# Kernel tuning notes

Hardware: AMD Instinct MI355X
Metric: run time of the kernel (lower is better)

## Reference

```python
import jax, jax.numpy as jnp
import numpy as np

N_NODES = 4096
N_EDGES = 8192
N_GRAPHS = 256
D_NODE = 64
D_EDGE = 32
H = 256


def setup_inputs() -> dict:
    key = jax.random.key(0)
    ks = jax.random.split(key, 16)
    s = lambda d: 1.0 / np.sqrt(d)
    inp = {
        "x": jax.random.normal(ks[0], (N_NODES, D_NODE), dtype=jnp.float32),
        "edge_index": jax.random.randint(ks[1], (2, N_EDGES), 0, N_NODES),
        "edge_attr": jax.random.normal(ks[2], (N_EDGES, D_EDGE), dtype=jnp.float32),
        "batch": jnp.sort(jax.random.randint(ks[3], (N_NODES,), 0, N_GRAPHS)),
        # conv1: edge MLP 32 -> 64*256, root weight 64->256, bias 256
        "nn1_w": jax.random.normal(ks[4], (D_EDGE, D_NODE * H), dtype=jnp.float32) * s(D_EDGE),
        "nn1_b": jnp.zeros((D_NODE * H,), dtype=jnp.float32),
        "root1_w": jax.random.normal(ks[5], (D_NODE, H), dtype=jnp.float32) * s(D_NODE),
        "bias1": jnp.zeros((H,), dtype=jnp.float32),
        # conv2: edge MLP 32 -> 256*256, root weight 256->256, bias 256
        "nn2_w": jax.random.normal(ks[6], (D_EDGE, H * H), dtype=jnp.float32) * s(D_EDGE),
        "nn2_b": jnp.zeros((H * H,), dtype=jnp.float32),
        "root2_w": jax.random.normal(ks[7], (H, H), dtype=jnp.float32) * s(H),
        "bias2": jnp.zeros((H,), dtype=jnp.float32),
        # readout MLP: 256 -> 128 -> 1
        "lin1_w": jax.random.normal(ks[8], (H, H // 2), dtype=jnp.float32) * s(H),
        "lin1_b": jnp.zeros((H // 2,), dtype=jnp.float32),
        "lin2_w": jax.random.normal(ks[9], (H // 2, 1), dtype=jnp.float32) * s(H // 2),
        "lin2_b": jnp.zeros((1,), dtype=jnp.float32),
    }
    return inp


def nnconv(x, src, dst, edge_attr, nn_w, nn_b, root_w, bias, out_c):
    # PyG NNConv (aggr='add'): per-edge weight matrix from edge MLP,
    # message = x[src] @ W_e, scatter-add at dst, plus root transform + bias.
    e = edge_attr.shape[0]
    in_c = x.shape[1]
    w_e = (edge_attr @ nn_w + nn_b).reshape(e, in_c, out_c)  # [E, in, out]
    msg = jnp.einsum('ei,eio->eo', x[src], w_e)              # [E, out]
    agg = jax.ops.segment_sum(msg, dst, num_segments=x.shape[0])
    return agg + x @ root_w + bias


def reference(x, edge_index, edge_attr, batch,
              nn1_w, nn1_b, root1_w, bias1,
              nn2_w, nn2_b, root2_w, bias2,
              lin1_w, lin1_b, lin2_w, lin2_b):
    src, dst = edge_index[0], edge_index[1]
    h = nnconv(x, src, dst, edge_attr, nn1_w, nn1_b, root1_w, bias1, H)
    h = jax.nn.relu(h)
    h = nnconv(h, src, dst, edge_attr, nn2_w, nn2_b, root2_w, bias2, H)
    # global mean pool over graphs
    sums = jax.ops.segment_sum(h, batch, num_segments=N_GRAPHS)
    cnts = jax.ops.segment_sum(jnp.ones((h.shape[0],), h.dtype), batch, num_segments=N_GRAPHS)
    pooled = sums / jnp.maximum(cnts, 1.0)[:, None]
    # dropout is identity in eval mode
    z = jax.nn.relu(pooled @ lin1_w + lin1_b)
    return jax.nn.sigmoid(z @ lin2_w + lin2_b)  # [N_GRAPHS, 1]
```

## Files before the change

kernel.cpp:

```cpp
#include <hip/hip_runtime.h>
#include <math.h>

#define N_NODES 4096
#define N_EDGES 8192
#define N_GRAPHS 256
#define D_NODE 64
#define D_EDGE 32
#define HH 256

#define K1 2176
#define K2 8704
#define NC1 34
#define NC2 136
#define NSL1 8
#define NSL3 32
#define CHUNK 64

typedef _Float16 half8v __attribute__((ext_vector_type(8)));
typedef _Float16 half4v __attribute__((ext_vector_type(4)));
typedef float floatx4 __attribute__((ext_vector_type(4)));

static const size_t OFF_S    = 0;
static const size_t OFF_BT1  = 17825792;
static const size_t OFF_BT2  = 18104320;
static const size_t OFF_CP   = 19218432;
static const size_t OFF_H    = 25509888;
static const size_t OFF_INT  = 26034176;
static const size_t OFF_POOL = 26050560;

__device__ void csr_body(const int* __restrict__ dst,
                         int* __restrict__ starts,
                         int* __restrict__ elist) {
    __shared__ int cnt[4096];
    __shared__ int ps[256];
    int t = threadIdx.x;
#pragma unroll
    for (int i = 0; i < 16; ++i) cnt[t * 16 + i] = 0;
    __syncthreads();
#pragma unroll
    for (int i = 0; i < 32; ++i) atomicAdd(&cnt[dst[i * 256 + t]], 1);
    __syncthreads();
    int v[16]; int s = 0;
#pragma unroll
    for (int i = 0; i < 16; ++i) { v[i] = cnt[t * 16 + i]; s += v[i]; }
    ps[t] = s;
    __syncthreads();
    for (int off = 1; off < 256; off <<= 1) {
        int tv = (t >= off) ? ps[t - off] : 0;
        __syncthreads();
        ps[t] += tv;
        __syncthreads();
    }
    int excl = ps[t] - s;
#pragma unroll
    for (int i = 0; i < 16; ++i) {
        starts[t * 16 + i] = excl;
        cnt[t * 16 + i] = excl;
        excl += v[i];
    }
    if (t == 255) starts[4096] = excl;
    __syncthreads();
#pragma unroll
    for (int i = 0; i < 32; ++i) {
        int e = i * 256 + t;
        int d = dst[e];
        int p = atomicAdd(&cnt[d], 1);
        elist[p] = e;
    }
}

__device__ void gstarts_body(const int* __restrict__ batch, int* __restrict__ gstarts) {
    int t = threadIdx.x;
    int lo = 0, hi = N_NODES;
    while (lo < hi) { int mid = (lo + hi) >> 1; if (batch[mid] < t) lo = mid + 1; else hi = mid; }
    gstarts[t] = lo;
    if (t == 0) gstarts[N_GRAPHS] = N_NODES;
}

__device__ void packT_body(const float* __restrict__ w,
                           const float* __restrict__ b,
                           const float* __restrict__ rw,
                           _Float16* __restrict__ BT,
                           int kk0, int o0, int K,
                           int wlim, int blim, int wshift, int wmask, int wrow) {
    __shared__ float T[64][65];
    int t = threadIdx.x;
    int ol = t & 63, kb = t >> 6;
#pragma unroll
    for (int p = 0; p < 16; ++p) {
        int kl = p * 4 + kb;
        int kk = kk0 + kl, o = o0 + ol;
        float v;
        if (kk < wlim)      v = w[(kk >> wshift) * wrow + (kk & wmask) * 256 + o];
        else if (kk < blim) v = b[(kk - wlim) * 256 + o];
        else                v = rw[(kk - blim) * 256 + o];
        T[kl][ol] = v;
    }
    __syncthreads();
    int kl2 = t & 63, ob = t >> 6;
#pragma unroll
    for (int p = 0; p < 16; ++p) {
        int ol2 = p * 4 + ob;
        BT[(size_t)(o0 + ol2) * K + kk0 + kl2] = (_Float16)T[kl2][ol2];
    }
}

__global__ __launch_bounds__(256) void prep_k(const int* __restrict__ dst,
                                              const int* __restrict__ batch,
                                              int* __restrict__ starts,
                                              int* __restrict__ elist,
                                              int* __restrict__ gstarts,
                                              const float* __restrict__ w1,
                                              const float* __restrict__ b1,
                                              const float* __restrict__ r1,
                                              const float* __restrict__ w2,
                                              const float* __restrict__ b2,
                                              const float* __restrict__ r2,
                                              _Float16* __restrict__ BT1,
                                              _Float16* __restrict__ BT2) {
    int bx = blockIdx.x, by = blockIdx.y;
    if (bx == 0) {
        if (by == 0) csr_body(dst, starts, elist);
        else if (by == 1) gstarts_body(batch, gstarts);
        return;
    }
    int pbx = bx - 1, o0 = by * 64;
    if (pbx < NC1)
        packT_body(w1, b1, r1, BT1, pbx * 64, o0, K1, 2048, 2112, 6, 63, 16384);
    else
        packT_body(w2, b2, r2, BT2, (pbx - NC1) * 64, o0, K2, 8192, 8448, 8, 255, 65536);
}

__global__ __launch_bounds__(256) void s1_k(const float* __restrict__ x,
                                            const float* __restrict__ ea,
                                            const int* __restrict__ src,
                                            const int* __restrict__ starts,
                                            const int* __restrict__ elist,
                                            _Float16* __restrict__ S) {
    int t = threadIdx.x;
    int n = blockIdx.x * 4 + (t >> 6);
    int tl = t & 63;
    int cg = tl & 7, kg = tl >> 3;
    int i0 = cg * 8;
    float acc[5][8] = {};
    int e0 = starts[n], e1 = starts[n + 1];
    for (int ie = e0; ie < e1; ++ie) {
        int e = elist[ie];
        int sn = src[e];
        float4 f0 = *(const float4*)&x[sn * 64 + i0];
        float4 f1 = *(const float4*)&x[sn * 64 + i0 + 4];
        float xv[8] = {f0.x, f0.y, f0.z, f0.w, f1.x, f1.y, f1.z, f1.w};
#pragma unroll
        for (int j = 0; j < 4; ++j) {
            float va = ea[e * 32 + kg + 8 * j];
#pragma unroll
            for (int c = 0; c < 8; ++c) acc[j][c] += va * xv[c];
        }
        if (kg == 0) {
#pragma unroll
            for (int c = 0; c < 8; ++c) acc[4][c] += xv[c];
        }
    }
    _Float16* row = S + (size_t)n * K1;
#pragma unroll
    for (int j = 0; j < 4; ++j) {
        int k = kg + 8 * j;
        half8v o;
#pragma unroll
        for (int c = 0; c < 8; ++c) o[c] = (_Float16)acc[j][c];
        *(half8v*)&row[k * 64 + i0] = o;
    }
    if (kg == 0) {
        half8v o;
#pragma unroll
        for (int c = 0; c < 8; ++c) o[c] = (_Float16)acc[4][c];
        *(half8v*)&row[32 * 64 + i0] = o;
    }
    if (kg == 1) {
        float4 f0 = *(const float4*)&x[n * 64 + i0];
        float4 f1 = *(const float4*)&x[n * 64 + i0 + 4];
        half8v o;
        o[0] = (_Float16)f0.x; o[1] = (_Float16)f0.y; o[2] = (_Float16)f0.z; o[3] = (_Float16)f0.w;
        o[4] = (_Float16)f1.x; o[5] = (_Float16)f1.y; o[6] = (_Float16)f1.z; o[7] = (_Float16)f1.w;
        *(half8v*)&row[2112 + i0] = o;
    }
}

__device__ __forceinline__ void async_copy16(const void* g, void* l) {
    __builtin_amdgcn_global_load_lds(
        (__attribute__((address_space(1))) unsigned int*)(g),
        (__attribute__((address_space(3))) unsigned int*)(l), 16, 0, 0);
}

__global__ __launch_bounds__(256, 3) void gemm_f16(const _Float16* __restrict__ A,
                                                   const _Float16* __restrict__ BT,
                                                   _Float16* __restrict__ Cpart,
                                                   int K, int NC, int Z) {
    __shared__ _Float16 lds[17408];
    _Float16* As = lds;
    _Float16* Bs = lds + 128 * 64;
    int tid = threadIdx.x;
    int w = tid >> 6, l = tid & 63;
    int mt = blockIdx.y, nt = blockIdx.x, z = blockIdx.z;
    int c0 = z * NC / Z, c1 = (z + 1) * NC / Z;
    int k0 = c0 * 64;
    int wm = w & 1, wn = w >> 1;

    int lr = l >> 3, lc = l & 7;
    int gc = lc ^ lr;
    const _Float16* gA0 = A  + (size_t)(mt * 128 + w * 32 + lr) * K + k0 + gc * 8;
    const _Float16* gB0 = BT + (size_t)(nt * 128 + w * 32 + lr) * K + k0 + gc * 8;

    int lm = l & 15, q4 = l >> 4;
    int sw = lm & 7;

    floatx4 acc[4][4] = {};

    for (int s = c0; s < c1; ++s) {
#pragma unroll
        for (int q = 0; q < 4; ++q) {
            async_copy16(gA0 + (size_t)q * 8 * K, As + (w * 32 + q * 8) * 64);
            async_copy16(gB0 + (size_t)q * 8 * K, Bs + (w * 32 + q * 8) * 64);
        }
        gA0 += 64; gB0 += 64;
        __syncthreads();
#pragma unroll
        for (int kw = 0; kw < 2; ++kw) {
            int ck = ((kw * 4 + q4) ^ sw) * 8;
            half8v af[4], bf[4];
#pragma unroll
            for (int i = 0; i < 4; ++i)
                af[i] = *(const half8v*)&As[(wm * 64 + i * 16 + lm) * 64 + ck];
#pragma unroll
            for (int j = 0; j < 4; ++j)
                bf[j] = *(const half8v*)&Bs[(wn * 64 + j * 16 + lm) * 64 + ck];
#pragma unroll
            for (int i = 0; i < 4; ++i)
#pragma unroll
                for (int j = 0; j < 4; ++j)
                    acc[i][j] = __builtin_amdgcn_mfma_f32_16x16x32_f16(af[i], bf[j], acc[i][j], 0, 0, 0);
        }
        __syncthreads();
    }

    _Float16* ep = lds + w * 4352;
#pragma unroll
    for (int i = 0; i < 4; ++i)
#pragma unroll
        for (int j = 0; j < 4; ++j)
#pragma unroll
            for (int r = 0; r < 4; ++r)
                ep[(i * 16 + q4 * 4 + r) * 68 + j * 16 + lm] = (_Float16)acc[i][j][r];
    __syncthreads();
    _Float16* Cp = Cpart + (size_t)z * (N_NODES * HH);
    int row8 = l >> 3, colg = (l & 7) * 8;
    int gm0 = mt * 128 + wm * 64, gn0 = nt * 128 + wn * 64;
#pragma unroll
    for (int i8 = 0; i8 < 8; ++i8) {
        int rr = i8 * 8 + row8;
        half4v lo = *(const half4v*)&ep[rr * 68 + colg];
        half4v hi = *(const half4v*)&ep[rr * 68 + colg + 4];
        half8v v;
        v[0] = lo[0]; v[1] = lo[1]; v[2] = lo[2]; v[3] = lo[3];
        v[4] = hi[0]; v[5] = hi[1]; v[6] = hi[2]; v[7] = hi[3];
        *(half8v*)&Cp[(size_t)(gm0 + rr) * HH + gn0 + colg] = v;
    }
}

__global__ __launch_bounds__(256) void hep_k(const _Float16* __restrict__ Cp,
                                             const float* __restrict__ bias,
                                             _Float16* __restrict__ h,
                                             float* __restrict__ pool) {
    if (blockIdx.x < 256) pool[blockIdx.x * 256 + threadIdx.x] = 0.f;
    int idx = (blockIdx.x * 256 + threadIdx.x) * 8;
    float a[8] = {};
#pragma unroll
    for (int zz = 0; zz < NSL1; ++zz) {
        half8v v = *(const half8v*)(Cp + (size_t)zz * (N_NODES * HH) + idx);
#pragma unroll
        for (int j = 0; j < 8; ++j) a[j] += (float)v[j];
    }
    int col = idx & 255;
    half8v o;
#pragma unroll
    for (int j = 0; j < 8; ++j) o[j] = (_Float16)fmaxf(a[j] + bias[col + j], 0.f);
    *(half8v*)(h + idx) = o;
}

__global__ __launch_bounds__(256) void sg_k(const _Float16* __restrict__ h,
                                            const float* __restrict__ ea,
                                            const int* __restrict__ src,
                                            const int* __restrict__ starts,
                                            const int* __restrict__ elist,
                                            const int* __restrict__ gstarts,
                                            _Float16* __restrict__ SG) {
    int g = blockIdx.x, ks = blockIdx.y, t = threadIdx.x;
    __shared__ int sl[CHUNK];
    __shared__ int el[CHUNK];
    __shared__ float eaS[CHUNK * 32];
    int nlo = gstarts[g], nhi = gstarts[g + 1];
    int e0 = starts[nlo], e1 = starts[nhi];
    _Float16* row = SG + (size_t)g * K2;
    int kbase = ks * 16;

    float acc[16] = {};
    float a32 = 0.f;
    for (int base = e0; base < e1; base += CHUNK) {
        int ne = min(CHUNK, e1 - base);
        if (t < ne) { int e = elist[base + t]; el[t] = e; sl[t] = src[e]; }
        __syncthreads();
        for (int j = t; j < ne * 32; j += 256)
            eaS[j] = ea[(size_t)el[j >> 5] * 32 + (j & 31)];
        __syncthreads();
        int ie = 0;
        for (; ie + 4 <= ne; ie += 4) {
            float hv[4];
#pragma unroll
            for (int u = 0; u < 4; ++u) hv[u] = (float)h[(size_t)sl[ie + u] * 256 + t];
#pragma unroll
            for (int u = 0; u < 4; ++u) {
                const float* er = &eaS[(ie + u) * 32 + kbase];
#pragma unroll
                for (int q = 0; q < 4; ++q) {
                    float4 ev = *(const float4*)&er[q * 4];
                    acc[q * 4 + 0] += ev.x * hv[u]; acc[q * 4 + 1] += ev.y * hv[u];
                    acc[q * 4 + 2] += ev.z * hv[u]; acc[q * 4 + 3] += ev.w * hv[u];
                }
                if (ks == 1) a32 += hv[u];
            }
        }
        for (; ie < ne; ++ie) {
            float hv = (float)h[(size_t)sl[ie] * 256 + t];
            const float* er = &eaS[ie * 32 + kbase];
#pragma unroll
            for (int q = 0; q < 4; ++q) {
                float4 ev = *(const float4*)&er[q * 4];
                acc[q * 4 + 0] += ev.x * hv; acc[q * 4 + 1] += ev.y * hv;
                acc[q * 4 + 2] += ev.z * hv; acc[q * 4 + 3] += ev.w * hv;
            }
            if (ks == 1) a32 += hv;
        }
        __syncthreads();
    }
#pragma unroll
    for (int j = 0; j < 16; ++j)
        row[(kbase + j) * 256 + t] = (_Float16)acc[j];
    if (ks == 1) {
        float aug = 0.f;
        int n = nlo;
        for (; n + 4 <= nhi; n += 4) {
            float hv[4];
#pragma unroll
            for (int u = 0; u < 4; ++u) hv[u] = (float)h[(size_t)(n + u) * 256 + t];
#pragma unroll
            for (int u = 0; u < 4; ++u) aug += hv[u];
        }
        for (; n < nhi; ++n) aug += (float)h[(size_t)n * 256 + t];
        row[32 * 256 + t] = (_Float16)a32;
        row[8448 + t] = (_Float16)aug;
    }
}

__global__ __launch_bounds__(256, 3) void gemm_sg(const _Float16* __restrict__ A,
                                                  const _Float16* __restrict__ BT,
                                                  float* __restrict__ pool,
                                                  int K, int NC, int Z) {
    __shared__ _Float16 lds[16384];
    _Float16* As = lds;
    _Float16* Bs = lds + 128 * 64;
    int tid = threadIdx.x;
    int w = tid >> 6, l = tid & 63;
    int mt = blockIdx.y, nt = blockIdx.x, z = blockIdx.z;
    int c0 = z * NC / Z, c1 = (z + 1) * NC / Z;
    int k0 = c0 * 64;
    int wm = w & 1, wn = w >> 1;

    int lr = l >> 3, lc = l & 7;
    int gc = lc ^ lr;
    const _Float16* gA0 = A  + (size_t)(mt * 128 + w * 32 + lr) * K + k0 + gc * 8;
    const _Float16* gB0 = BT + (size_t)(nt * 128 + w * 32 + lr) * K + k0 + gc * 8;

    int lm = l & 15, q4 = l >> 4;
    int sw = lm & 7;

    floatx4 acc[4][4] = {};

    for (int s = c0; s < c1; ++s) {
#pragma unroll
        for (int q = 0; q < 4; ++q) {
            async_copy16(gA0 + (size_t)q * 8 * K, As + (w * 32 + q * 8) * 64);
            async_copy16(gB0 + (size_t)q * 8 * K, Bs + (w * 32 + q * 8) * 64);
        }
        gA0 += 64; gB0 += 64;
        __syncthreads();
#pragma unroll
        for (int kw = 0; kw < 2; ++kw) {
            int ck = ((kw * 4 + q4) ^ sw) * 8;
            half8v af[4], bf[4];
#pragma unroll
            for (int i = 0; i < 4; ++i)
                af[i] = *(const half8v*)&As[(wm * 64 + i * 16 + lm) * 64 + ck];
#pragma unroll
            for (int j = 0; j < 4; ++j)
                bf[j] = *(const half8v*)&Bs[(wn * 64 + j * 16 + lm) * 64 + ck];
#pragma unroll
            for (int i = 0; i < 4; ++i)
#pragma unroll
                for (int j = 0; j < 4; ++j)
                    acc[i][j] = __builtin_amdgcn_mfma_f32_16x16x32_f16(af[i], bf[j], acc[i][j], 0, 0, 0);
        }
        __syncthreads();
    }

    int gm0 = mt * 128 + wm * 64, gn0 = nt * 128 + wn * 64;
#pragma unroll
    for (int i = 0; i < 4; ++i)
#pragma unroll
        for (int j = 0; j < 4; ++j)
#pragma unroll
            for (int r = 0; r < 4; ++r)
                atomicAdd(&pool[(size_t)(gm0 + i * 16 + q4 * 4 + r) * HH + gn0 + j * 16 + lm],
                          acc[i][j][r]);
}

__global__ __launch_bounds__(256) void readout_k(const float* __restrict__ pool,
                                                 const int* __restrict__ gstarts,
                                                 const float* __restrict__ bias2,
                                                 const float* __restrict__ l1w,
                                                 const float* __restrict__ l1b,
                                                 const float* __restrict__ l2w,
                                                 const float* __restrict__ l2b,
                                                 float* __restrict__ out) {
    int g = blockIdx.x, t = threadIdx.x;
    __shared__ float sp[256];
    __shared__ float sz[128];
    int lo = gstarts[g], hi = gstarts[g + 1];
    sp[t] = (hi > lo) ? (pool[g * 256 + t] / (float)(hi - lo) + bias2[t]) : 0.f;
    __syncthreads();
    if (t < 128) {
        float a = l1b[t];
#pragma unroll 8
        for (int i = 0; i < 256; ++i) a += sp[i] * l1w[i * 128 + t];
        sz[t] = fmaxf(a, 0.f) * l2w[t];
    }
    __syncthreads();
    for (int ss = 64; ss > 0; ss >>= 1) {
        if (t < ss) sz[t] += sz[t + ss];
        __syncthreads();
    }
    if (t == 0) {
        float zz = sz[0] + l2b[0];
        out[g] = 1.0f / (1.0f + expf(-zz));
    }
}

extern "C" void kernel_launch(void* const* d_in, const int* in_sizes, int n_in,
                              void* d_out, int out_size, void* d_ws, size_t ws_size,
                              hipStream_t stream) {
    const float* x       = (const float*)d_in[0];
    const int*   ei      = (const int*)d_in[1];
    const float* ea      = (const float*)d_in[2];
    const int*   batch   = (const int*)d_in[3];
    const float* nn1_w   = (const float*)d_in[4];
    const float* nn1_b   = (const float*)d_in[5];
    const float* root1_w = (const float*)d_in[6];
    const float* bias1   = (const float*)d_in[7];
    const float* nn2_w   = (const float*)d_in[8];
    const float* nn2_b   = (const float*)d_in[9];
    const float* root2_w = (const float*)d_in[10];
    const float* bias2   = (const float*)d_in[11];
    const float* lin1_w  = (const float*)d_in[12];
    const float* lin1_b  = (const float*)d_in[13];
    const float* lin2_w  = (const float*)d_in[14];
    const float* lin2_b  = (const float*)d_in[15];
    float* out = (float*)d_out;
    float* ws  = (float*)d_ws;

    _Float16* S   = (_Float16*)(ws + OFF_S);
    _Float16* BT1 = (_Float16*)(ws + OFF_BT1);
    _Float16* BT2 = (_Float16*)(ws + OFF_BT2);
    _Float16* Cp  = (_Float16*)(ws + OFF_CP);
    _Float16* h   = (_Float16*)(ws + OFF_H);
    int* ip      = (int*)(ws + OFF_INT);
    int* starts  = ip;
    int* elist   = ip + 4100;
    int* gstarts = ip + 12292;
    float* pool  = ws + OFF_POOL;

    const int* srcv = ei;
    const int* dstv = ei + N_EDGES;

    prep_k<<<dim3(1 + NC1 + NC2, 4), 256, 0, stream>>>(
        dstv, batch, starts, elist, gstarts,
        nn1_w, nn1_b, root1_w, nn2_w, nn2_b, root2_w, BT1, BT2);

    s1_k<<<1024, 256, 0, stream>>>(x, ea, srcv, starts, elist, S);

    gemm_f16<<<dim3(2, 32, NSL1), 256, 0, stream>>>(S, BT1, Cp, K1, NC1, NSL1);

    hep_k<<<512, 256, 0, stream>>>(Cp, bias1, h, pool);

    sg_k<<<dim3(N_GRAPHS, 2), 256, 0, stream>>>(h, ea, srcv, starts, elist, gstarts, S);

    gemm_sg<<<dim3(2, 2, NSL3), 256, 0, stream>>>(S, BT2, pool, K2, NC2, NSL3);

    readout_k<<<N_GRAPHS, 256, 0, stream>>>(pool, gstarts, bias2,
                                            lin1_w, lin1_b, lin2_w, lin2_b, out);
}
```

Before: 168.4 us.

## Reduce conv1 split-K partials with fp32 atomics instead of fp16 partial buffers

```diff
diff --git a/kernel.cpp b/kernel.cpp
--- a/kernel.cpp
+++ b/kernel.cpp
@@ -13,7 +13,7 @@
 #define NC1 34
 #define NC2 136
 #define NSL1 8
-#define NSL3 32
+#define NSL3 64
 #define CHUNK 64
 
 typedef _Float16 half8v __attribute__((ext_vector_type(8)));
@@ -23,7 +23,7 @@
 static const size_t OFF_S    = 0;
 static const size_t OFF_BT1  = 17825792;
 static const size_t OFF_BT2  = 18104320;
-static const size_t OFF_CP   = 19218432;
+static const size_t OFF_H32  = 19218432;
 static const size_t OFF_H    = 25509888;
 static const size_t OFF_INT  = 26034176;
 static const size_t OFF_POOL = 26050560;
@@ -136,8 +136,12 @@
                                             const int* __restrict__ src,
                                             const int* __restrict__ starts,
                                             const int* __restrict__ elist,
-                                            _Float16* __restrict__ S) {
+                                            _Float16* __restrict__ S,
+                                            float* __restrict__ H32) {
     int t = threadIdx.x;
+    floatx4 z4 = {0.f, 0.f, 0.f, 0.f};
+    *(floatx4*)&H32[(size_t)(blockIdx.x * 256 + t) * 4] = z4;
+
     int n = blockIdx.x * 4 + (t >> 6);
     int tl = t & 63;
     int cg = tl & 7, kg = tl >> 3;
@@ -194,9 +198,9 @@
 
 __global__ __launch_bounds__(256, 3) void gemm_f16(const _Float16* __restrict__ A,
                                                    const _Float16* __restrict__ BT,
-                                                   _Float16* __restrict__ Cpart,
+                                                   float* __restrict__ H32,
                                                    int K, int NC, int Z) {
-    __shared__ _Float16 lds[17408];
+    __shared__ _Float16 lds[16384];
     _Float16* As = lds;
     _Float16* Bs = lds + 128 * 64;
     int tid = threadIdx.x;
@@ -243,43 +247,26 @@
         __syncthreads();
     }
 
-    _Float16* ep = lds + w * 4352;
+    int gm0 = mt * 128 + wm * 64, gn0 = nt * 128 + wn * 64;
 #pragma unroll
     for (int i = 0; i < 4; ++i)
 #pragma unroll
         for (int j = 0; j < 4; ++j)
 #pragma unroll
             for (int r = 0; r < 4; ++r)
-                ep[(i * 16 + q4 * 4 + r) * 68 + j * 16 + lm] = (_Float16)acc[i][j][r];
-    __syncthreads();
-    _Float16* Cp = Cpart + (size_t)z * (N_NODES * HH);
-    int row8 = l >> 3, colg = (l & 7) * 8;
-    int gm0 = mt * 128 + wm * 64, gn0 = nt * 128 + wn * 64;
-#pragma unroll
-    for (int i8 = 0; i8 < 8; ++i8) {
-        int rr = i8 * 8 + row8;
-        half4v lo = *(const half4v*)&ep[rr * 68 + colg];
-        half4v hi = *(const half4v*)&ep[rr * 68 + colg + 4];
-        half8v v;
-        v[0] = lo[0]; v[1] = lo[1]; v[2] = lo[2]; v[3] = lo[3];
-        v[4] = hi[0]; v[5] = hi[1]; v[6] = hi[2]; v[7] = hi[3];
-        *(half8v*)&Cp[(size_t)(gm0 + rr) * HH + gn0 + colg] = v;
-    }
-}
-
-__global__ __launch_bounds__(256) void hep_k(const _Float16* __restrict__ Cp,
+                atomicAdd(&H32[(size_t)(gm0 + i * 16 + q4 * 4 + r) * HH + gn0 + j * 16 + lm],
+                          acc[i][j][r]);
+}
+
+__global__ __launch_bounds__(256) void hep_k(const float* __restrict__ H32,
                                              const float* __restrict__ bias,
                                              _Float16* __restrict__ h,
                                              float* __restrict__ pool) {
     if (blockIdx.x < 256) pool[blockIdx.x * 256 + threadIdx.x] = 0.f;
     int idx = (blockIdx.x * 256 + threadIdx.x) * 8;
-    float a[8] = {};
-#pragma unroll
-    for (int zz = 0; zz < NSL1; ++zz) {
-        half8v v = *(const half8v*)(Cp + (size_t)zz * (N_NODES * HH) + idx);
-#pragma unroll
-        for (int j = 0; j < 8; ++j) a[j] += (float)v[j];
-    }
+    float4 a0 = *(const float4*)&H32[idx];
+    float4 a1 = *(const float4*)&H32[idx + 4];
+    float a[8] = {a0.x, a0.y, a0.z, a0.w, a1.x, a1.y, a1.z, a1.w};
     int col = idx & 255;
     half8v o;
 #pragma unroll
@@ -479,7 +466,7 @@
     _Float16* S   = (_Float16*)(ws + OFF_S);
     _Float16* BT1 = (_Float16*)(ws + OFF_BT1);
     _Float16* BT2 = (_Float16*)(ws + OFF_BT2);
-    _Float16* Cp  = (_Float16*)(ws + OFF_CP);
+    float*    H32 = ws + OFF_H32;
     _Float16* h   = (_Float16*)(ws + OFF_H);
     int* ip      = (int*)(ws + OFF_INT);
     int* starts  = ip;
@@ -494,11 +481,11 @@
         dstv, batch, starts, elist, gstarts,
         nn1_w, nn1_b, root1_w, nn2_w, nn2_b, root2_w, BT1, BT2);
 
-    s1_k<<<1024, 256, 0, stream>>>(x, ea, srcv, starts, elist, S);
-
-    gemm_f16<<<dim3(2, 32, NSL1), 256, 0, stream>>>(S, BT1, Cp, K1, NC1, NSL1);
-
-    hep_k<<<512, 256, 0, stream>>>(Cp, bias1, h, pool);
+    s1_k<<<1024, 256, 0, stream>>>(x, ea, srcv, starts, elist, S, H32);
+
+    gemm_f16<<<dim3(2, 32, NSL1), 256, 0, stream>>>(S, BT1, H32, K1, NC1, NSL1);
+
+    hep_k<<<512, 256, 0, stream>>>(H32, bias1, h, pool);
 
     sg_k<<<dim3(N_GRAPHS, 2), 256, 0, stream>>>(h, ea, srcv, starts, elist, gstarts, S);
 
```

Result: slower. 192.7 us (+14.4%).
